# Kernel tuning notes

Hardware: AMD Instinct MI355X
Metric: run time of the kernel (lower is better)

Reference implementation:

```python
import jax, jax.numpy as jnp
import numpy as np

N, C_IN, C_OUT, K = 100000, 64, 64, 16
E = N * K
BN_EPS = 1e-5


def setup_inputs() -> dict:
    key = jax.random.key(0)
    ks = jax.random.split(key, 4)
    x = jax.random.normal(ks[0], (N, C_IN), dtype=jnp.float32)
    # knn-style edge list: each node i is the center (row) of exactly K edges
    edge_row = jnp.repeat(jnp.arange(N, dtype=jnp.int64), K)
    edge_col = jax.random.randint(ks[1], (E,), 0, N).astype(jnp.int64)
    W1 = jax.random.normal(ks[2], (2 * C_IN, C_OUT), dtype=jnp.float32) * (1.0 / np.sqrt(2 * C_IN))
    W2 = jax.random.normal(ks[3], (C_OUT, C_OUT), dtype=jnp.float32) * (1.0 / np.sqrt(C_OUT))
    return {
        'x': x, 'edge_row': edge_row, 'edge_col': edge_col,
        'W1': W1, 'b1': jnp.zeros((C_OUT,), jnp.float32),
        'g1': jnp.ones((C_OUT,), jnp.float32), 'be1': jnp.zeros((C_OUT,), jnp.float32),
        'W2': W2, 'b2': jnp.zeros((C_OUT,), jnp.float32),
        'g2': jnp.ones((C_OUT,), jnp.float32), 'be2': jnp.zeros((C_OUT,), jnp.float32),
    }


def _bn(h, gamma, beta):
    # BatchNorm1d in training mode: biased batch stats over the edge dim
    mean = jnp.mean(h, axis=0)
    var = jnp.mean(jnp.square(h - mean), axis=0)
    return (h - mean) * jax.lax.rsqrt(var + BN_EPS) * gamma + beta


def reference(x, edge_row, edge_col, W1, b1, g1, be1, W2, b2, g2, be2):
    xi = x[edge_row]                      # [E, C_in]  gather (center)
    xj = x[edge_col]                      # [E, C_in]  gather (neighbor)
    feat = jnp.concatenate([xi, xj - xi], axis=1)   # [E, 2*C_in]
    h = jax.nn.relu(_bn(feat @ W1 + b1, g1, be1))   # [E, C_out]
    h = jax.nn.relu(_bn(h @ W2 + b2, g2, be2))      # [E, C_out]
    # scatter-max back to nodes; every node has K edges so no empty segments
    out = jax.ops.segment_max(h, edge_row, num_segments=x.shape[0])
    return out
```

## Files before the change

kernel.cpp:

```cpp
#include <hip/hip_runtime.h>


#define N_NODES 100000
#define KE 16
#define E_EDGES (N_NODES * KE)
#define BN_EPS 1e-5f
#define NCHUNK (N_NODES / KE)

typedef __attribute__((ext_vector_type(8))) short bf16x8;
typedef __attribute__((ext_vector_type(4))) float f32x4;
typedef __attribute__((ext_vector_type(4))) int i32x4;

#define MFMA(a, b, c) __builtin_amdgcn_mfma_f32_16x16x32_bf16((a), (b), (c), 0, 0, 0)

static __device__ __forceinline__ short bf16b(float f) {
  __bf16 h = (__bf16)f;
  return __builtin_bit_cast(short, h);
}

#if __has_builtin(__builtin_amdgcn_cvt_pk_bf16_f32)
static __device__ __forceinline__ int pk2(float a, float b) {
  return __builtin_bit_cast(int, __builtin_amdgcn_cvt_pk_bf16_f32(a, b));
}
#else
static __device__ __forceinline__ int pk2(float a, float b) {
  return (int)(unsigned short)bf16b(a) | ((int)(unsigned short)bf16b(b) << 16);
}
#endif

static __device__ __forceinline__ bf16x8 pack8(float4 a, float4 b) {
  i32x4 v = {pk2(a.x, a.y), pk2(a.z, a.w), pk2(b.x, b.y), pk2(b.z, b.w)};
  return __builtin_bit_cast(bf16x8, v);
}

static __device__ __forceinline__ float bf2f(short s) {
  unsigned u = ((unsigned)(unsigned short)s) << 16;
  return __builtin_bit_cast(float, u);
}

__global__ __launch_bounds__(256) void k_cvt(const float* __restrict__ x,
                                             short* __restrict__ xb) {
  int g = blockIdx.x * 256 + threadIdx.x;
  const float4* x4 = (const float4*)x;
  float4 f0 = x4[2 * g], f1 = x4[2 * g + 1];
  bf16x8 v = pack8(f0, f1);
  *(bf16x8*)(xb + g * 8) = v;
}

__global__ void pack_w(const float* __restrict__ W1, const float* __restrict__ W2,
                       short* __restrict__ wp1, short* __restrict__ wp2) {
  int tid = blockIdx.x * blockDim.x + threadIdx.x;
  if (tid < 1024) {
    int l = tid & 63, st = tid >> 6;
    int s = st >> 2, t = st & 3;
    int quad = l >> 4, n16 = l & 15;
    for (int j = 0; j < 8; j++) {
      int k = 32 * s + quad * 8 + j, c = 16 * t + n16;
      float w = (s < 2) ? (W1[k * 64 + c] - W1[(k + 64) * 64 + c])
                        : W1[k * 64 + c];
      wp1[tid * 8 + j] = bf16b(w);
    }
  } else if (tid < 1536) {
    int e = tid - 1024;
    int l = e & 63, st = e >> 6;
    int s = st >> 2, t = st & 3;
    int quad = l >> 4, n16 = l & 15;
    for (int j = 0; j < 8; j++) {
      int k = 32 * s + quad * 8 + j, c = 16 * t + n16;
      wp2[e * 8 + j] = bf16b(W2[k * 64 + c]);
    }
  }
}

static __device__ __forceinline__ void stat_acc(const f32x4 acc[4], float sacc[4],
                                                float qacc[4]) {
#pragma unroll
  for (int t = 0; t < 4; t++) {
    sacc[t] += (acc[t][0] + acc[t][1]) + (acc[t][2] + acc[t][3]);
    qacc[t] = fmaf(acc[t][0], acc[t][0],
              fmaf(acc[t][1], acc[t][1],
              fmaf(acc[t][2], acc[t][2],
              fmaf(acc[t][3], acc[t][3], qacc[t]))));
  }
}

static __device__ __forceinline__ void stat_flush(float sacc[4], float qacc[4],
                                                  int quad, int n16, float* lstat) {
#pragma unroll
  for (int t = 0; t < 4; t++) {
    float s = sacc[t], q = qacc[t];
    s += __shfl_xor(s, 16); s += __shfl_xor(s, 32);
    q += __shfl_xor(q, 16); q += __shfl_xor(q, 32);
    if (quad == 0) {
      atomicAdd(&lstat[16 * t + n16], s);
      atomicAdd(&lstat[64 + 16 * t + n16], q);
    }
  }
}

__global__ __launch_bounds__(256, 4) void k_pass1(const short* __restrict__ xb,
                                                  const int* __restrict__ ecol,
                                                  const bf16x8* __restrict__ wp1,
                                                  float* __restrict__ gacc) {
  __shared__ float lstat[128];
  __shared__ int eblk[256];
  __shared__ __align__(16) short xit[1024];
  __shared__ __align__(16) short wfl[8192];
  int tid = threadIdx.x;
  if (tid < 128) lstat[tid] = 0.f;
  int nb = blockIdx.x * 16;
  eblk[tid] = ecol[nb * KE + tid];
  if (tid < 128)
    *(bf16x8*)(&xit[tid * 8]) = ((const bf16x8*)(xb + (size_t)nb * 64))[tid];
#pragma unroll
  for (int r = 0; r < 4; r++)
    ((bf16x8*)wfl)[r * 256 + tid] = wp1[r * 256 + tid];
  __syncthreads();
  int wave = tid >> 6, l = tid & 63, quad = l >> 4, n16 = l & 15;
  const bf16x8* wf = (const bf16x8*)wfl;
  bf16x8 j0[4], j1[4];
#pragma unroll
  for (int v = 0; v < 4; v++) {
    int idx = eblk[(wave * 4 + v) * 16 + n16];
    const short* pj = xb + (size_t)idx * 64 + quad * 8;
    j0[v] = *(const bf16x8*)pj;
    j1[v] = *(const bf16x8*)(pj + 32);
  }
  float sacc[4] = {0.f, 0.f, 0.f, 0.f}, qacc[4] = {0.f, 0.f, 0.f, 0.f};
#pragma unroll
  for (int v = 0; v < 4; v++) {
    int p = wave * 4 + v;
    bf16x8 xi0 = *(const bf16x8*)(&xit[p * 64 + quad * 8]);
    bf16x8 xi1 = *(const bf16x8*)(&xit[p * 64 + 32 + quad * 8]);
    f32x4 acc[4];
#pragma unroll
    for (int t = 0; t < 4; t++) {
      f32x4 a = {0.f, 0.f, 0.f, 0.f};
      a = MFMA(xi0, wf[(0 + t) * 64 + l], a);
      a = MFMA(xi1, wf[(4 + t) * 64 + l], a);
      a = MFMA(j0[v], wf[(8 + t) * 64 + l], a);
      a = MFMA(j1[v], wf[(12 + t) * 64 + l], a);
      acc[t] = a;
    }
    stat_acc(acc, sacc, qacc);
  }
  stat_flush(sacc, qacc, quad, n16, lstat);
  __syncthreads();
  if (tid < 128) atomicAdd(&gacc[(blockIdx.x & 63) * 128 + tid], lstat[tid]);
}

__global__ void k_finalize(const float* __restrict__ gacc, const float* __restrict__ g,
                           const float* __restrict__ be, float* __restrict__ bn) {
  int c = threadIdx.x;
  float s = 0.f, q = 0.f;
  for (int i = 0; i < 64; i++) {
    s += gacc[i * 128 + c];
    q += gacc[i * 128 + 64 + c];
  }
  float mean = s * (1.0f / E_EDGES);
  float var = q * (1.0f / E_EDGES) - mean * mean;
  float rstd = rsqrtf(var + BN_EPS);
  float a = g[c] * rstd;
  bn[c] = a;
  bn[64 + c] = be[c] - mean * a;
}

__global__ __launch_bounds__(256, 3) void k_pass2(const short* __restrict__ xb,
                                                  const int* __restrict__ ecol,
                                                  const bf16x8* __restrict__ wp1,
                                                  const bf16x8* __restrict__ wp2,
                                                  const float* __restrict__ bn1,
                                                  float* __restrict__ gacc,
                                                  short* __restrict__ hmax,
                                                  short* __restrict__ hmin) {
  __shared__ float lstat[128];
  __shared__ int eblk[256];
  __shared__ __align__(16) short xit[1024];
  __shared__ __align__(16) short wfl[8192];
  __shared__ __align__(16) short tiles[4][16 * 72];
  int tid = threadIdx.x;
  if (tid < 128) lstat[tid] = 0.f;
  int nb = blockIdx.x * 16;
  eblk[tid] = ecol[nb * KE + tid];
  if (tid < 128)
    *(bf16x8*)(&xit[tid * 8]) = ((const bf16x8*)(xb + (size_t)nb * 64))[tid];
#pragma unroll
  for (int r = 0; r < 4; r++)
    ((bf16x8*)wfl)[r * 256 + tid] = wp1[r * 256 + tid];
  __syncthreads();
  int wave = tid >> 6, l = tid & 63, quad = l >> 4, n16 = l & 15;
  const bf16x8* wf = (const bf16x8*)wfl;
  bf16x8 wf2[8];
#pragma unroll
  for (int u = 0; u < 8; u++) wf2[u] = wp2[u * 64 + l];
  float a1c[4], b1c[4];
#pragma unroll
  for (int t = 0; t < 4; t++) {
    a1c[t] = bn1[16 * t + n16];
    b1c[t] = bn1[64 + 16 * t + n16];
  }
  bf16x8 j0[4], j1[4];
#pragma unroll
  for (int v = 0; v < 4; v++) {
    int idx = eblk[(wave * 4 + v) * 16 + n16];
    const short* pj = xb + (size_t)idx * 64 + quad * 8;
    j0[v] = *(const bf16x8*)pj;
    j1[v] = *(const bf16x8*)(pj + 32);
  }
  float sacc[4] = {0.f, 0.f, 0.f, 0.f}, qacc[4] = {0.f, 0.f, 0.f, 0.f};
  short* myt = &tiles[wave][0];
#pragma unroll
  for (int v = 0; v < 4; v++) {
    int p = wave * 4 + v;
    bf16x8 xi0 = *(const bf16x8*)(&xit[p * 64 + quad * 8]);
    bf16x8 xi1 = *(const bf16x8*)(&xit[p * 64 + 32 + quad * 8]);
    f32x4 acc1[4];
#pragma unroll
    for (int t = 0; t < 4; t++) {
      f32x4 a = {0.f, 0.f, 0.f, 0.f};
      a = MFMA(xi0, wf[(0 + t) * 64 + l], a);
      a = MFMA(xi1, wf[(4 + t) * 64 + l], a);
      a = MFMA(j0[v], wf[(8 + t) * 64 + l], a);
      a = MFMA(j1[v], wf[(12 + t) * 64 + l], a);
      acc1[t] = a;
    }
#pragma unroll
    for (int t = 0; t < 4; t++) {
      int c = 16 * t + n16;
#pragma unroll
      for (int r = 0; r < 4; r++) {
        float h = fmaxf(fmaf(acc1[t][r], a1c[t], b1c[t]), 0.f);
        myt[(quad * 4 + r) * 72 + c] = bf16b(h);
      }
    }
    bf16x8 f0 = *(bf16x8*)(myt + n16 * 72 + quad * 8);
    bf16x8 f1 = *(bf16x8*)(myt + n16 * 72 + 32 + quad * 8);
    f32x4 acc2[4];
#pragma unroll
    for (int t = 0; t < 4; t++) {
      f32x4 a = {0.f, 0.f, 0.f, 0.f};
      a = MFMA(f0, wf2[0 + t], a);
      a = MFMA(f1, wf2[4 + t], a);
      acc2[t] = a;
    }
    stat_acc(acc2, sacc, qacc);
    float vmx[4], vmn[4];
#pragma unroll
    for (int t = 0; t < 4; t++) {
      float mx = fmaxf(fmaxf(acc2[t][0], acc2[t][1]), fmaxf(acc2[t][2], acc2[t][3]));
      float mn = fminf(fminf(acc2[t][0], acc2[t][1]), fminf(acc2[t][2], acc2[t][3]));
      mx = fmaxf(mx, __shfl_xor(mx, 16)); mx = fmaxf(mx, __shfl_xor(mx, 32));
      mn = fminf(mn, __shfl_xor(mn, 16)); mn = fminf(mn, __shfl_xor(mn, 32));
      vmx[t] = mx; vmn[t] = mn;
    }
    int n = nb + p;
    float ox = (quad == 0) ? vmx[0] : (quad == 1) ? vmx[1] : (quad == 2) ? vmx[2] : vmx[3];
    float on = (quad == 0) ? vmn[0] : (quad == 1) ? vmn[1] : (quad == 2) ? vmn[2] : vmn[3];
    hmax[(size_t)n * 64 + l] = bf16b(ox);
    hmin[(size_t)n * 64 + l] = bf16b(on);
  }
  stat_flush(sacc, qacc, quad, n16, lstat);
  __syncthreads();
  if (tid < 128) atomicAdd(&gacc[(blockIdx.x & 63) * 128 + tid], lstat[tid]);
}

__global__ __launch_bounds__(256) void k_pass3(const short* __restrict__ hmax,
                                               const short* __restrict__ hmin,
                                               const float* __restrict__ bn2,
                                               float* __restrict__ out) {
  int g = blockIdx.x * 256 + threadIdx.x;
  int base = g * 4;
  int c4 = base & 63;
  short4 mx4 = *(const short4*)(hmax + base);
  short4 mn4 = *(const short4*)(hmin + base);
  float4 a4 = *(const float4*)(bn2 + c4);
  float4 b4 = *(const float4*)(bn2 + 64 + c4);
  float4 o;
  o.x = fmaxf(a4.x >= 0.f ? fmaf(a4.x, bf2f(mx4.x), b4.x) : fmaf(a4.x, bf2f(mn4.x), b4.x), 0.f);
  o.y = fmaxf(a4.y >= 0.f ? fmaf(a4.y, bf2f(mx4.y), b4.y) : fmaf(a4.y, bf2f(mn4.y), b4.y), 0.f);
  o.z = fmaxf(a4.z >= 0.f ? fmaf(a4.z, bf2f(mx4.z), b4.z) : fmaf(a4.z, bf2f(mn4.z), b4.z), 0.f);
  o.w = fmaxf(a4.w >= 0.f ? fmaf(a4.w, bf2f(mx4.w), b4.w) : fmaf(a4.w, bf2f(mn4.w), b4.w), 0.f);
  *(float4*)(out + base) = o;
}

extern "C" void kernel_launch(void* const* d_in, const int* in_sizes, int n_in,
                              void* d_out, int out_size, void* d_ws, size_t ws_size,
                              hipStream_t stream) {
  const float* x   = (const float*)d_in[0];
  const int*   ec  = (const int*)d_in[2];
  const float* W1  = (const float*)d_in[3];
  const float* g1  = (const float*)d_in[5];
  const float* be1 = (const float*)d_in[6];
  const float* W2  = (const float*)d_in[7];
  const float* g2  = (const float*)d_in[9];
  const float* be2 = (const float*)d_in[10];
  float* out = (float*)d_out;

  char* ws = (char*)d_ws;
  bf16x8* wp1  = (bf16x8*)(ws);
  bf16x8* wp2  = (bf16x8*)(ws + 16384);
  float* gacc1 = (float*)(ws + 24576);
  float* gacc2 = (float*)(ws + 57344);
  float* bn1   = (float*)(ws + 90112);
  float* bn2   = (float*)(ws + 90624);
  short* xb    = (short*)(ws + 98304);
  short* hmax  = (short*)(ws + 98304 + 12800000);
  short* hmin  = (short*)(ws + 98304 + 2 * 12800000);

  hipMemsetAsync(gacc1, 0, 65536, stream);

  hipLaunchKernelGGL(pack_w, dim3(6), dim3(256), 0, stream, W1, W2,
                     (short*)wp1, (short*)wp2);
  hipLaunchKernelGGL(k_cvt, dim3(3125), dim3(256), 0, stream, x, xb);
  hipLaunchKernelGGL(k_pass1, dim3(NCHUNK), dim3(256), 0, stream,
                     xb, ec, wp1, gacc1);
  hipLaunchKernelGGL(k_finalize, dim3(1), dim3(64), 0, stream, gacc1, g1, be1, bn1);
  hipLaunchKernelGGL(k_pass2, dim3(NCHUNK), dim3(256), 0, stream,
                     xb, ec, wp1, wp2, bn1, gacc2, hmax, hmin);
  hipLaunchKernelGGL(k_finalize, dim3(1), dim3(64), 0, stream, gacc2, g2, be2, bn2);
  hipLaunchKernelGGL(k_pass3, dim3(6250), dim3(256), 0, stream, hmax, hmin, bn2, out);
}
```

Measured before the change: 245.8 us.

## Merge prep kernels, fold BN finalize into consumers, shrink stat slots, raise occupancy

Merges the weight-packing and x-to-bf16 conversion kernels into one launch. Removes the two single-block BN finalize kernels by having every block of pass2 and pass3 recompute the mean and scale from the global accumulators into shared memory. Global stat slots drop from 64 to 16, which shrinks the memset and the per-block reduction, and the launch-bounds occupancy hints for pass1 and pass2 are raised. The trade-offs are redundant finalize reads in thousands of blocks, more atomic contention per slot, and possible register spilling from the tighter launch bounds.

After: 492.8 us. +100.4%, slower.

```diff
diff --git a/kernel.cpp b/kernel.cpp
--- a/kernel.cpp
+++ b/kernel.cpp
@@ -6,6 +6,7 @@
 #define E_EDGES (N_NODES * KE)
 #define BN_EPS 1e-5f
 #define NCHUNK (N_NODES / KE)
+#define GSLOTS 16
 
 typedef __attribute__((ext_vector_type(8))) short bf16x8;
 typedef __attribute__((ext_vector_type(4))) float f32x4;
@@ -38,18 +39,20 @@
   return __builtin_bit_cast(float, u);
 }
 
-__global__ __launch_bounds__(256) void k_cvt(const float* __restrict__ x,
-                                             short* __restrict__ xb) {
-  int g = blockIdx.x * 256 + threadIdx.x;
-  const float4* x4 = (const float4*)x;
-  float4 f0 = x4[2 * g], f1 = x4[2 * g + 1];
-  bf16x8 v = pack8(f0, f1);
-  *(bf16x8*)(xb + g * 8) = v;
-}
-
-__global__ void pack_w(const float* __restrict__ W1, const float* __restrict__ W2,
-                       short* __restrict__ wp1, short* __restrict__ wp2) {
-  int tid = blockIdx.x * blockDim.x + threadIdx.x;
+__global__ __launch_bounds__(256) void k_prep(const float* __restrict__ x,
+                                              short* __restrict__ xb,
+                                              const float* __restrict__ W1,
+                                              const float* __restrict__ W2,
+                                              short* __restrict__ wp1,
+                                              short* __restrict__ wp2) {
+  if (blockIdx.x < 3125) {
+    int g = blockIdx.x * 256 + threadIdx.x;
+    const float4* x4 = (const float4*)x;
+    float4 f0 = x4[2 * g], f1 = x4[2 * g + 1];
+    *(bf16x8*)(xb + g * 8) = pack8(f0, f1);
+    return;
+  }
+  int tid = (blockIdx.x - 3125) * 256 + threadIdx.x;
   if (tid < 1024) {
     int l = tid & 63, st = tid >> 6;
     int s = st >> 2, t = st & 3;
@@ -98,7 +101,27 @@
   }
 }
 
-__global__ __launch_bounds__(256, 4) void k_pass1(const short* __restrict__ xb,
+static __device__ __forceinline__ void bn_finalize(const float* __restrict__ gacc,
+                                                   const float* __restrict__ g,
+                                                   const float* __restrict__ be,
+                                                   float* lbn, int tid) {
+  if (tid < 64) {
+    float s = 0.f, q = 0.f;
+#pragma unroll
+    for (int i = 0; i < GSLOTS; i++) {
+      s += gacc[i * 128 + tid];
+      q += gacc[i * 128 + 64 + tid];
+    }
+    float mean = s * (1.0f / E_EDGES);
+    float var = q * (1.0f / E_EDGES) - mean * mean;
+    float rstd = rsqrtf(var + BN_EPS);
+    float a = g[tid] * rstd;
+    lbn[tid] = a;
+    lbn[64 + tid] = be[tid] - mean * a;
+  }
+}
+
+__global__ __launch_bounds__(256, 6) void k_pass1(const short* __restrict__ xb,
                                                   const int* __restrict__ ecol,
                                                   const bf16x8* __restrict__ wp1,
                                                   float* __restrict__ gacc) {
@@ -146,40 +169,29 @@
   }
   stat_flush(sacc, qacc, quad, n16, lstat);
   __syncthreads();
-  if (tid < 128) atomicAdd(&gacc[(blockIdx.x & 63) * 128 + tid], lstat[tid]);
-}
-
-__global__ void k_finalize(const float* __restrict__ gacc, const float* __restrict__ g,
-                           const float* __restrict__ be, float* __restrict__ bn) {
-  int c = threadIdx.x;
-  float s = 0.f, q = 0.f;
-  for (int i = 0; i < 64; i++) {
-    s += gacc[i * 128 + c];
-    q += gacc[i * 128 + 64 + c];
-  }
-  float mean = s * (1.0f / E_EDGES);
-  float var = q * (1.0f / E_EDGES) - mean * mean;
-  float rstd = rsqrtf(var + BN_EPS);
-  float a = g[c] * rstd;
-  bn[c] = a;
-  bn[64 + c] = be[c] - mean * a;
-}
-
-__global__ __launch_bounds__(256, 3) void k_pass2(const short* __restrict__ xb,
+  if (tid < 128)
+    atomicAdd(&gacc[(blockIdx.x & (GSLOTS - 1)) * 128 + tid], lstat[tid]);
+}
+
+__global__ __launch_bounds__(256, 5) void k_pass2(const short* __restrict__ xb,
                                                   const int* __restrict__ ecol,
                                                   const bf16x8* __restrict__ wp1,
                                                   const bf16x8* __restrict__ wp2,
-                                                  const float* __restrict__ bn1,
+                                                  const float* __restrict__ gacc1,
+                                                  const float* __restrict__ g1,
+                                                  const float* __restrict__ be1,
                                                   float* __restrict__ gacc,
                                                   short* __restrict__ hmax,
                                                   short* __restrict__ hmin) {
   __shared__ float lstat[128];
+  __shared__ float lbn[128];
   __shared__ int eblk[256];
   __shared__ __align__(16) short xit[1024];
   __shared__ __align__(16) short wfl[8192];
   __shared__ __align__(16) short tiles[4][16 * 72];
   int tid = threadIdx.x;
   if (tid < 128) lstat[tid] = 0.f;
+  bn_finalize(gacc1, g1, be1, lbn, tid);
   int nb = blockIdx.x * 16;
   eblk[tid] = ecol[nb * KE + tid];
   if (tid < 128)
@@ -196,8 +208,8 @@
   float a1c[4], b1c[4];
 #pragma unroll
   for (int t = 0; t < 4; t++) {
-    a1c[t] = bn1[16 * t + n16];
-    b1c[t] = bn1[64 + 16 * t + n16];
+    a1c[t] = lbn[16 * t + n16];
+    b1c[t] = lbn[64 + 16 * t + n16];
   }
   bf16x8 j0[4], j1[4];
 #pragma unroll
@@ -261,20 +273,27 @@
   }
   stat_flush(sacc, qacc, quad, n16, lstat);
   __syncthreads();
-  if (tid < 128) atomicAdd(&gacc[(blockIdx.x & 63) * 128 + tid], lstat[tid]);
+  if (tid < 128)
+    atomicAdd(&gacc[(blockIdx.x & (GSLOTS - 1)) * 128 + tid], lstat[tid]);
 }
 
 __global__ __launch_bounds__(256) void k_pass3(const short* __restrict__ hmax,
                                                const short* __restrict__ hmin,
-                                               const float* __restrict__ bn2,
+                                               const float* __restrict__ gacc2,
+                                               const float* __restrict__ g2,
+                                               const float* __restrict__ be2,
                                                float* __restrict__ out) {
-  int g = blockIdx.x * 256 + threadIdx.x;
+  __shared__ float lbn[128];
+  int tid = threadIdx.x;
+  bn_finalize(gacc2, g2, be2, lbn, tid);
+  __syncthreads();
+  int g = blockIdx.x * 256 + tid;
   int base = g * 4;
   int c4 = base & 63;
   short4 mx4 = *(const short4*)(hmax + base);
   short4 mn4 = *(const short4*)(hmin + base);
-  float4 a4 = *(const float4*)(bn2 + c4);
-  float4 b4 = *(const float4*)(bn2 + 64 + c4);
+  float4 a4 = *(const float4*)(&lbn[c4]);
+  float4 b4 = *(const float4*)(&lbn[64 + c4]);
   float4 o;
   o.x = fmaxf(a4.x >= 0.f ? fmaf(a4.x, bf2f(mx4.x), b4.x) : fmaf(a4.x, bf2f(mn4.x), b4.x), 0.f);
   o.y = fmaxf(a4.y >= 0.f ? fmaf(a4.y, bf2f(mx4.y), b4.y) : fmaf(a4.y, bf2f(mn4.y), b4.y), 0.f);
@@ -300,23 +319,19 @@
   bf16x8* wp1  = (bf16x8*)(ws);
   bf16x8* wp2  = (bf16x8*)(ws + 16384);
   float* gacc1 = (float*)(ws + 24576);
-  float* gacc2 = (float*)(ws + 57344);
-  float* bn1   = (float*)(ws + 90112);
-  float* bn2   = (float*)(ws + 90624);
+  float* gacc2 = (float*)(ws + 32768);
   short* xb    = (short*)(ws + 98304);
   short* hmax  = (short*)(ws + 98304 + 12800000);
   short* hmin  = (short*)(ws + 98304 + 2 * 12800000);
 
-  hipMemsetAsync(gacc1, 0, 65536, stream);
-
-  hipLaunchKernelGGL(pack_w, dim3(6), dim3(256), 0, stream, W1, W2,
-                     (short*)wp1, (short*)wp2);
-  hipLaunchKernelGGL(k_cvt, dim3(3125), dim3(256), 0, stream, x, xb);
+  hipMemsetAsync(gacc1, 0, 16384, stream);
+
+  hipLaunchKernelGGL(k_prep, dim3(3131), dim3(256), 0, stream, x, xb,
+                     W1, W2, (short*)wp1, (short*)wp2);
   hipLaunchKernelGGL(k_pass1, dim3(NCHUNK), dim3(256), 0, stream,
                      xb, ec, wp1, gacc1);
-  hipLaunchKernelGGL(k_finalize, dim3(1), dim3(64), 0, stream, gacc1, g1, be1, bn1);
   hipLaunchKernelGGL(k_pass2, dim3(NCHUNK), dim3(256), 0, stream,
-                     xb, ec, wp1, wp2, bn1, gacc2, hmax, hmin);
-  hipLaunchKernelGGL(k_finalize, dim3(1), dim3(64), 0, stream, gacc2, g2, be2, bn2);
-  hipLaunchKernelGGL(k_pass3, dim3(6250), dim3(256), 0, stream, hmax, hmin, bn2, out);
-}
+                     xb, ec, wp1, wp2, gacc1, g1, be1, gacc2, hmax, hmin);
+  hipLaunchKernelGGL(k_pass3, dim3(6250), dim3(256), 0, stream,
+                     hmax, hmin, gacc2, g2, be2, out);
+}
```
